# Kernel tuning notes

Measured on AMD Instinct MI355X. Metric: run time of the kernel, lower is better.

## Reference

```python
import jax, jax.numpy as jnp
import numpy as np

N = 262144        # tokens routed
D = 1024          # input_dim
E = 64            # num_experts
TOP_K = 2
NOISE_EPS = 1e-05
ALPHA = 10.0


def setup_inputs() -> dict:
    key = jax.random.key(0)
    k1, k2, k3, k4, k5 = jax.random.split(key, 5)
    x = jax.random.normal(k1, (N, D), dtype=jnp.float32)
    # nn.Linear init scale ~ 1/sqrt(fan_in); keep logits at sane magnitude
    gate_w = jax.random.normal(k2, (E, D), dtype=jnp.float32) * (1.0 / np.sqrt(D))
    gate_b = jax.random.normal(k3, (E,), dtype=jnp.float32) * 0.01
    # w_noise is initialized to zeros in the module; use small random values
    # so the noise path is exercised
    w_noise = jax.random.normal(k4, (E, E), dtype=jnp.float32) * 0.01
    noise = jax.random.normal(k5, (N, E), dtype=jnp.float32)  # torch.randn_like
    return {"x": x, "gate_w": gate_w, "gate_b": gate_b,
            "w_noise": w_noise, "noise": noise}


def reference(x, gate_w, gate_b, w_noise, noise):
    # gate linear: [N, D] @ [D, E] + [E]
    clean_logits = jnp.einsum('nd,ed->ne', x, gate_w) + gate_b
    # training-mode learnable noise injection
    raw_noise_stddev = clean_logits @ w_noise                 # [N, E]
    noise_stddev = jax.nn.softplus(raw_noise_stddev) + NOISE_EPS
    logits = clean_logits + noise * noise_stddev              # noisy_logits

    # decompostion_tp: k-th largest per row (kthvalue(n - k + 1) == k-th largest)
    kth_largest = jax.lax.top_k(logits, TOP_K)[0][:, -1]       # [N]
    mask = logits < kth_largest[:, None]                       # strictly below kth
    sm = jax.nn.softmax(logits, axis=1)
    out = jnp.where(mask,
                    ALPHA * jnp.log1p(sm),      # alpha * log(sm + 1)
                    ALPHA * jnp.expm1(sm))      # alpha * (exp(sm) - 1)

    gates = jax.nn.softmax(out, axis=1)
    return gates
```

## Files before the change

### kernel.cpp

```cpp
#include <hip/hip_runtime.h>

typedef _Float16 half8v __attribute__((ext_vector_type(8)));
typedef float f32x4 __attribute__((ext_vector_type(4)));

constexpr float INV4096 = 1.0f / 4096.0f;
constexpr float ALPHA = 10.0f;

__device__ __forceinline__ f32x4 mfma16(half8v a, half8v b, f32x4 c_) {
  return __builtin_amdgcn_mfma_f32_16x16x32_f16(a, b, c_, 0, 0, 0);
}

__device__ __forceinline__ void dma16(const void *g, void *l) {
  __builtin_amdgcn_global_load_lds(
      (const __attribute__((address_space(1))) void *)g,
      (__attribute__((address_space(3))) void *)l, 16, 0, 0);
}

__global__ __launch_bounds__(256) void presplit(const float *__restrict__ GW,
                                                const float *__restrict__ WN,
                                                char *__restrict__ ws) {
  const int b = blockIdx.x;
  const int tid = threadIdx.x;
  if (b < 64) {
    int idx = b * 256 + tid;
    int e = idx >> 8;
    int c4 = idx & 255;
    f32x4 v = *reinterpret_cast<const f32x4 *>(GW + (size_t)idx * 4);
#pragma unroll
    for (int j = 0; j < 4; ++j) {
      int k = c4 * 4 + j;
      float vv = v[j];
      _Float16 hh = (_Float16)vv;
      _Float16 ll = (_Float16)((vv - (float)hh) * 4096.0f);
      int ck = k >> 6, kk = k & 63;
      int off = ck * 16384 + e * 128 + ((((kk >> 3) ^ (e & 7))) << 4) + ((kk & 7) << 1);
      *reinterpret_cast<_Float16 *>(ws + off) = hh;
      *reinterpret_cast<_Float16 *>(ws + off + 8192) = ll;
    }
  } else {
    int idx = (b - 64) * 256 + tid;
    int k = idx >> 4;
    int e0 = (idx & 15) << 2;
    f32x4 v = *reinterpret_cast<const f32x4 *>(WN + (size_t)k * 64 + e0);
#pragma unroll
    for (int j = 0; j < 4; ++j) {
      int e = e0 + j;
      float vv = v[j];
      _Float16 hh = (_Float16)vv;
      _Float16 ll = (_Float16)((vv - (float)hh) * 4096.0f);
      int off = 262144 + e * 128 + ((((k >> 3) ^ (e & 7))) << 4) + ((k & 7) << 1);
      *reinterpret_cast<_Float16 *>(ws + off) = hh;
      *reinterpret_cast<_Float16 *>(ws + off + 8192) = ll;
    }
  }
}

__global__ __launch_bounds__(256, 3) void topk_gating(
    const float *__restrict__ X, const char *__restrict__ WS,
    const float *__restrict__ GB, const float *__restrict__ NZ,
    float *__restrict__ OUT) {
  __shared__ __align__(16) char lds[32768];
  const int tid = threadIdx.x;
  const int lane = tid & 63;
  const int wv = tid >> 6;
  const int q = lane >> 4;
  const int c = lane & 15;
  const int waveRow = blockIdx.x * 64 + wv * 16;

  f32x4 accH[4] = {};
  f32x4 accX[4] = {};
  f32x4 aCur[4], aNxt[4];

  const float *xBase = X + (size_t)(waveRow + c) * 1024 + q * 8;
  aCur[0] = *(const f32x4 *)(xBase + 0);
  aCur[1] = *(const f32x4 *)(xBase + 4);
  aCur[2] = *(const f32x4 *)(xBase + 32);
  aCur[3] = *(const f32x4 *)(xBase + 36);
#pragma unroll
  for (int i = 0; i < 4; ++i)
    dma16(WS + i * 4096 + wv * 1024 + lane * 16, lds + i * 4096 + wv * 1024);
  __syncthreads();

  for (int kc = 0; kc < 16; ++kc) {
    if (kc < 15) {
      const float *xb = xBase + (kc + 1) * 64;
      aNxt[0] = *(const f32x4 *)(xb + 0);
      aNxt[1] = *(const f32x4 *)(xb + 4);
      aNxt[2] = *(const f32x4 *)(xb + 32);
      aNxt[3] = *(const f32x4 *)(xb + 36);
      const int wbuf = ((kc + 1) & 1) * 16384;
      const char *src = WS + (kc + 1) * 16384;
#pragma unroll
      for (int i = 0; i < 4; ++i)
        dma16(src + i * 4096 + wv * 1024 + lane * 16,
              lds + wbuf + i * 4096 + wv * 1024);
    }
    const int buf = (kc & 1) * 16384;
#pragma unroll
    for (int ks = 0; ks < 2; ++ks) {
      half8v ah, al;
#pragma unroll
      for (int j = 0; j < 8; ++j) {
        float xv = aCur[ks * 2 + (j >> 2)][j & 3];
        _Float16 hh = (_Float16)xv;
        ah[j] = hh;
        al[j] = (_Float16)((xv - (float)hh) * 4096.0f);
      }
#pragma unroll
      for (int t = 0; t < 4; ++t) {
        int e = t * 16 + c;
        int off = buf + e * 128 + ((((ks * 4 + q) ^ (e & 7))) << 4);
        half8v bh = *reinterpret_cast<half8v *>(lds + off);
        half8v bl = *reinterpret_cast<half8v *>(lds + off + 8192);
        accH[t] = mfma16(ah, bh, accH[t]);
        accX[t] = mfma16(ah, bl, accX[t]);
        accX[t] = mfma16(al, bh, accX[t]);
      }
    }
    if (kc < 15) {
#pragma unroll
      for (int i = 0; i < 4; ++i) aCur[i] = aNxt[i];
    }
    __syncthreads();
  }

  float nz[4][4];
#pragma unroll
  for (int t = 0; t < 4; ++t)
#pragma unroll
    for (int r = 0; r < 4; ++r)
      nz[t][r] = NZ[(size_t)(waveRow + 4 * q + r) * 64 + t * 16 + c];

#pragma unroll
  for (int i = 0; i < 4; ++i)
    dma16(WS + 262144 + i * 4096 + wv * 1024 + lane * 16,
          lds + i * 4096 + wv * 1024);

  float cl[4][4];
#pragma unroll
  for (int t = 0; t < 4; ++t) {
    float bs = GB[t * 16 + c];
#pragma unroll
    for (int r = 0; r < 4; ++r)
      cl[t][r] = accH[t][r] + accX[t][r] * INV4096 + bs;
  }

  char *cb = lds + 16384 + wv * 4096;
#pragma unroll
  for (int t = 0; t < 4; ++t)
#pragma unroll
    for (int r = 0; r < 4; ++r) {
      int row = 4 * q + r;
      int colf = t * 16 + c;
      int off = row * 256 + ((((colf >> 2) ^ row)) << 4) + ((colf & 3) << 2);
      *reinterpret_cast<float *>(cb + off) = cl[t][r];
    }
  __syncthreads();

  f32x4 rH[4] = {};
  f32x4 rX[4] = {};
#pragma unroll
  for (int ks = 0; ks < 2; ++ks) {
    int slot0 = ks * 8 + q * 2;
    f32x4 a0 = *reinterpret_cast<f32x4 *>(cb + c * 256 + (((slot0 ^ c)) << 4));
    f32x4 a1 = *reinterpret_cast<f32x4 *>(cb + c * 256 + ((((slot0 + 1) ^ c)) << 4));
    half8v ah, al;
#pragma unroll
    for (int j = 0; j < 4; ++j) {
      float v = a0[j];
      _Float16 hh = (_Float16)v;
      ah[j] = hh;
      al[j] = (_Float16)((v - (float)hh) * 4096.0f);
      float v2 = a1[j];
      _Float16 h2 = (_Float16)v2;
      ah[4 + j] = h2;
      al[4 + j] = (_Float16)((v2 - (float)h2) * 4096.0f);
    }
#pragma unroll
    for (int t = 0; t < 4; ++t) {
      int e = t * 16 + c;
      int off = e * 128 + ((((ks * 4 + q) ^ (e & 7))) << 4);
      half8v bh = *reinterpret_cast<half8v *>(lds + off);
      half8v bl = *reinterpret_cast<half8v *>(lds + off + 8192);
      rH[t] = mfma16(ah, bh, rH[t]);
      rX[t] = mfma16(ah, bl, rX[t]);
      rX[t] = mfma16(al, bh, rX[t]);
    }
  }

  float lg[4][4];
#pragma unroll
  for (int t = 0; t < 4; ++t)
#pragma unroll
    for (int r = 0; r < 4; ++r) {
      float raw = rH[t][r] + rX[t][r] * INV4096;
      float sp = fmaxf(raw, 0.0f) + __logf(1.0f + __expf(-fabsf(raw)));
      lg[r][t] = cl[t][r] + nz[t][r] * (sp + 1e-5f);
    }

#pragma unroll
  for (int r = 0; r < 4; ++r) {
    float v0 = lg[r][0], v1 = lg[r][1], v2 = lg[r][2], v3 = lg[r][3];
    float a = fmaxf(v0, v1), b_ = fminf(v0, v1);
    float d1 = fmaxf(v2, v3), d2 = fminf(v2, v3);
    float m1 = fmaxf(a, d1);
    float m2 = fmaxf(fminf(a, d1), fmaxf(b_, d2));
#pragma unroll
    for (int s = 1; s <= 8; s <<= 1) {
      float om1 = __shfl_xor(m1, s, 64);
      float om2 = __shfl_xor(m2, s, 64);
      float hi = fmaxf(m1, om1);
      float lo = fminf(m1, om1);
      float sec = (m1 >= om1) ? m2 : om2;
      m2 = fmaxf(lo, sec);
      m1 = hi;
    }
    float se[4], ssum = 0.f;
#pragma unroll
    for (int t = 0; t < 4; ++t) {
      se[t] = __expf(lg[r][t] - m1);
      ssum += se[t];
    }
#pragma unroll
    for (int s = 1; s <= 8; s <<= 1) ssum += __shfl_xor(ssum, s, 64);
    float inv = 1.0f / ssum;
    float ov[4];
#pragma unroll
    for (int t = 0; t < 4; ++t) {
      float sm = se[t] * inv;
      float vlog = ALPHA * __logf(1.0f + sm);
      float vexp = ALPHA * (__expf(sm) - 1.0f);
      ov[t] = (lg[r][t] < m2) ? vlog : vexp;
    }
    float g = fmaxf(fmaxf(ov[0], ov[1]), fmaxf(ov[2], ov[3]));
#pragma unroll
    for (int s = 1; s <= 8; s <<= 1) g = fmaxf(g, __shfl_xor(g, s, 64));
    float gsum = 0.f;
#pragma unroll
    for (int t = 0; t < 4; ++t) {
      ov[t] = __expf(ov[t] - g);
      gsum += ov[t];
    }
#pragma unroll
    for (int s = 1; s <= 8; s <<= 1) gsum += __shfl_xor(gsum, s, 64);
    float ginv = 1.0f / gsum;
    size_t rowOff = (size_t)(waveRow + 4 * q + r) * 64;
#pragma unroll
    for (int t = 0; t < 4; ++t)
      OUT[rowOff + t * 16 + c] = ov[t] * ginv;
  }
}

extern "C" void kernel_launch(void *const *d_in, const int *in_sizes, int n_in,
                              void *d_out, int out_size, void *d_ws,
                              size_t ws_size, hipStream_t stream) {
  const float *x = (const float *)d_in[0];
  const float *gw = (const float *)d_in[1];
  const float *gb = (const float *)d_in[2];
  const float *wn = (const float *)d_in[3];
  const float *nz = (const float *)d_in[4];
  float *out = (float *)d_out;
  char *ws = (char *)d_ws;
  const int N = in_sizes[0] / 1024;

  hipLaunchKernelGGL(presplit, dim3(68), dim3(256), 0, stream, gw, wn, ws);
  hipLaunchKernelGGL(topk_gating, dim3(N / 64), dim3(256), 0, stream, x, ws,
                     gb, nz, out);
}
```

Baseline: 283.3 us.

## Deepen GEMM pipeline to triple-buffered LDS with explicit vmcnt waits

Replaces the double-buffered K loop with a fully unrolled three-stage pipeline. Weight chunks are DMA'd into LDS two steps ahead and X rows are prefetched three steps ahead into rotating register banks. The __syncthreads calls become raw s_barrier plus hand-counted s_waitcnt vmcnt so more loads stay in flight. This aims to hide global-memory latency in the memory-bound X stream. In exchange LDS grows to 48KB and register pressure rises, which may reduce occupancy, and the hand-counted vmcnt values are fragile if the compiler reorders loads.

```diff
diff --git a/kernel.cpp b/kernel.cpp
--- a/kernel.cpp
+++ b/kernel.cpp
@@ -9,11 +9,13 @@
 __device__ __forceinline__ f32x4 mfma16(half8v a, half8v b, f32x4 c_) {
   return __builtin_amdgcn_mfma_f32_16x16x32_f16(a, b, c_, 0, 0, 0);
 }
-
 __device__ __forceinline__ void dma16(const void *g, void *l) {
   __builtin_amdgcn_global_load_lds(
       (const __attribute__((address_space(1))) void *)g,
       (__attribute__((address_space(3))) void *)l, 16, 0, 0);
+}
+template <int N> __device__ __forceinline__ void wait_vm() {
+  asm volatile("s_waitcnt vmcnt(%0)" ::"n"(N) : "memory");
 }
 
 __global__ __launch_bounds__(256) void presplit(const float *__restrict__ GW,
@@ -59,7 +61,7 @@
     const float *__restrict__ X, const char *__restrict__ WS,
     const float *__restrict__ GB, const float *__restrict__ NZ,
     float *__restrict__ OUT) {
-  __shared__ __align__(16) char lds[32768];
+  __shared__ __align__(16) char lds[49152];
   const int tid = threadIdx.x;
   const int lane = tid & 63;
   const int wv = tid >> 6;
@@ -69,61 +71,88 @@
 
   f32x4 accH[4] = {};
   f32x4 accX[4] = {};
-  f32x4 aCur[4], aNxt[4];
+  f32x4 a0[4], a1[4], a2[4];
 
   const float *xBase = X + (size_t)(waveRow + c) * 1024 + q * 8;
-  aCur[0] = *(const f32x4 *)(xBase + 0);
-  aCur[1] = *(const f32x4 *)(xBase + 4);
-  aCur[2] = *(const f32x4 *)(xBase + 32);
-  aCur[3] = *(const f32x4 *)(xBase + 36);
+  const char *wsL = WS + wv * 1024 + lane * 16;
+  char *ldsL = lds + wv * 1024;
+
+#define LDA4(dst, p)                        \
+  {                                         \
+    dst[0] = *(const f32x4 *)((p) + 0);     \
+    dst[1] = *(const f32x4 *)((p) + 4);     \
+    dst[2] = *(const f32x4 *)((p) + 32);    \
+    dst[3] = *(const f32x4 *)((p) + 36);    \
+  }
+#define DMAB(CK)                                                            \
+  {                                                                         \
+    _Pragma("unroll") for (int i_ = 0; i_ < 4; ++i_)                        \
+        dma16(wsL + (CK) * 16384 + i_ * 4096,                               \
+              ldsL + ((CK) % 3) * 16384 + i_ * 4096);                       \
+  }
+#define CONV(A, ah, al)                                           \
+  {                                                               \
+    _Pragma("unroll") for (int ks_ = 0; ks_ < 2; ++ks_)           \
+        _Pragma("unroll") for (int j_ = 0; j_ < 8; ++j_) {        \
+      float xv_ = A[ks_ * 2 + (j_ >> 2)][j_ & 3];                 \
+      _Float16 hh_ = (_Float16)xv_;                               \
+      ah[ks_][j_] = hh_;                                          \
+      al[ks_][j_] = (_Float16)((xv_ - (float)hh_) * 4096.0f);     \
+    }                                                             \
+  }
+#define MFMAB(BUF, ah, al)                                                 \
+  {                                                                        \
+    _Pragma("unroll") for (int ks_ = 0; ks_ < 2; ++ks_)                    \
+        _Pragma("unroll") for (int t_ = 0; t_ < 4; ++t_) {                 \
+      int e_ = t_ * 16 + c;                                                \
+      int off_ = (BUF) + e_ * 128 + ((((ks_ * 4 + q) ^ (e_ & 7))) << 4);   \
+      half8v bh_ = *reinterpret_cast<half8v *>(lds + off_);                \
+      half8v bl_ = *reinterpret_cast<half8v *>(lds + off_ + 8192);         \
+      accH[t_] = mfma16(ah[ks_], bh_, accH[t_]);                           \
+      accX[t_] = mfma16(ah[ks_], bl_, accX[t_]);                           \
+      accX[t_] = mfma16(al[ks_], bh_, accX[t_]);                           \
+    }                                                                      \
+  }
+#define STEP(KC, ABANK)                                          \
+  {                                                              \
+    half8v ah[2], al[2];                                         \
+    CONV(ABANK, ah, al);                                         \
+    if ((KC) + 2 <= 15) DMAB((KC) + 2);                          \
+    if ((KC) + 3 <= 15) LDA4(ABANK, xBase + ((KC) + 3) * 64);    \
+    MFMAB(((KC) % 3) * 16384, ah, al);                           \
+  }
+#define BAR() __builtin_amdgcn_s_barrier()
+
+  DMAB(0);
+  DMAB(1);
+  LDA4(a0, xBase);
+  LDA4(a1, xBase + 64);
+  LDA4(a2, xBase + 128);
+  wait_vm<16>();
+  BAR();
+
+  STEP(0, a0)  wait_vm<12>(); BAR();
+  STEP(1, a1)  wait_vm<12>(); BAR();
+  STEP(2, a2)  wait_vm<12>(); BAR();
+  STEP(3, a0)  wait_vm<12>(); BAR();
+  STEP(4, a1)  wait_vm<12>(); BAR();
+  STEP(5, a2)  wait_vm<12>(); BAR();
+  STEP(6, a0)  wait_vm<12>(); BAR();
+  STEP(7, a1)  wait_vm<12>(); BAR();
+  STEP(8, a2)  wait_vm<12>(); BAR();
+  STEP(9, a0)  wait_vm<12>(); BAR();
+  STEP(10, a1) wait_vm<12>(); BAR();
+  STEP(11, a2) wait_vm<12>(); BAR();
+  STEP(12, a0) wait_vm<12>(); BAR();
+  STEP(13, a1) wait_vm<8>();  BAR();
+  STEP(14, a2) wait_vm<0>();  BAR();
+  STEP(15, a0)
+
+  float bs0 = GB[c], bs1 = GB[16 + c], bs2 = GB[32 + c], bs3 = GB[48 + c];
 #pragma unroll
   for (int i = 0; i < 4; ++i)
-    dma16(WS + i * 4096 + wv * 1024 + lane * 16, lds + i * 4096 + wv * 1024);
-  __syncthreads();
-
-  for (int kc = 0; kc < 16; ++kc) {
-    if (kc < 15) {
-      const float *xb = xBase + (kc + 1) * 64;
-      aNxt[0] = *(const f32x4 *)(xb + 0);
-      aNxt[1] = *(const f32x4 *)(xb + 4);
-      aNxt[2] = *(const f32x4 *)(xb + 32);
-      aNxt[3] = *(const f32x4 *)(xb + 36);
-      const int wbuf = ((kc + 1) & 1) * 16384;
-      const char *src = WS + (kc + 1) * 16384;
-#pragma unroll
-      for (int i = 0; i < 4; ++i)
-        dma16(src + i * 4096 + wv * 1024 + lane * 16,
-              lds + wbuf + i * 4096 + wv * 1024);
-    }
-    const int buf = (kc & 1) * 16384;
-#pragma unroll
-    for (int ks = 0; ks < 2; ++ks) {
-      half8v ah, al;
-#pragma unroll
-      for (int j = 0; j < 8; ++j) {
-        float xv = aCur[ks * 2 + (j >> 2)][j & 3];
-        _Float16 hh = (_Float16)xv;
-        ah[j] = hh;
-        al[j] = (_Float16)((xv - (float)hh) * 4096.0f);
-      }
-#pragma unroll
-      for (int t = 0; t < 4; ++t) {
-        int e = t * 16 + c;
-        int off = buf + e * 128 + ((((ks * 4 + q) ^ (e & 7))) << 4);
-        half8v bh = *reinterpret_cast<half8v *>(lds + off);
-        half8v bl = *reinterpret_cast<half8v *>(lds + off + 8192);
-        accH[t] = mfma16(ah, bh, accH[t]);
-        accX[t] = mfma16(ah, bl, accX[t]);
-        accX[t] = mfma16(al, bh, accX[t]);
-      }
-    }
-    if (kc < 15) {
-#pragma unroll
-      for (int i = 0; i < 4; ++i) aCur[i] = aNxt[i];
-    }
-    __syncthreads();
-  }
-
+    dma16(wsL + 262144 + i * 4096, ldsL + 16384 + i * 4096);
+  asm volatile("" ::: "memory");
   float nz[4][4];
 #pragma unroll
   for (int t = 0; t < 4; ++t)
@@ -131,21 +160,15 @@
     for (int r = 0; r < 4; ++r)
       nz[t][r] = NZ[(size_t)(waveRow + 4 * q + r) * 64 + t * 16 + c];
 
-#pragma unroll
-  for (int i = 0; i < 4; ++i)
-    dma16(WS + 262144 + i * 4096 + wv * 1024 + lane * 16,
-          lds + i * 4096 + wv * 1024);
-
   float cl[4][4];
-#pragma unroll
-  for (int t = 0; t < 4; ++t) {
-    float bs = GB[t * 16 + c];
+  const float bsv[4] = {bs0, bs1, bs2, bs3};
+#pragma unroll
+  for (int t = 0; t < 4; ++t)
 #pragma unroll
     for (int r = 0; r < 4; ++r)
-      cl[t][r] = accH[t][r] + accX[t][r] * INV4096 + bs;
-  }
-
-  char *cb = lds + 16384 + wv * 4096;
+      cl[t][r] = accH[t][r] + accX[t][r] * INV4096 + bsv[t];
+
+  char *cb = lds + 32768 + wv * 4096;
 #pragma unroll
   for (int t = 0; t < 4; ++t)
 #pragma unroll
@@ -155,23 +178,24 @@
       int off = row * 256 + ((((colf >> 2) ^ row)) << 4) + ((colf & 3) << 2);
       *reinterpret_cast<float *>(cb + off) = cl[t][r];
     }
-  __syncthreads();
+  wait_vm<16>();
+  BAR();
 
   f32x4 rH[4] = {};
   f32x4 rX[4] = {};
 #pragma unroll
   for (int ks = 0; ks < 2; ++ks) {
     int slot0 = ks * 8 + q * 2;
-    f32x4 a0 = *reinterpret_cast<f32x4 *>(cb + c * 256 + (((slot0 ^ c)) << 4));
-    f32x4 a1 = *reinterpret_cast<f32x4 *>(cb + c * 256 + ((((slot0 + 1) ^ c)) << 4));
+    f32x4 va = *reinterpret_cast<f32x4 *>(cb + c * 256 + (((slot0 ^ c)) << 4));
+    f32x4 vb = *reinterpret_cast<f32x4 *>(cb + c * 256 + ((((slot0 + 1) ^ c)) << 4));
     half8v ah, al;
 #pragma unroll
     for (int j = 0; j < 4; ++j) {
-      float v = a0[j];
+      float v = va[j];
       _Float16 hh = (_Float16)v;
       ah[j] = hh;
       al[j] = (_Float16)((v - (float)hh) * 4096.0f);
-      float v2 = a1[j];
+      float v2 = vb[j];
       _Float16 h2 = (_Float16)v2;
       ah[4 + j] = h2;
       al[4 + j] = (_Float16)((v2 - (float)h2) * 4096.0f);
@@ -179,7 +203,7 @@
 #pragma unroll
     for (int t = 0; t < 4; ++t) {
       int e = t * 16 + c;
-      int off = e * 128 + ((((ks * 4 + q) ^ (e & 7))) << 4);
+      int off = 16384 + e * 128 + ((((ks * 4 + q) ^ (e & 7))) << 4);
       half8v bh = *reinterpret_cast<half8v *>(lds + off);
       half8v bl = *reinterpret_cast<half8v *>(lds + off + 8192);
       rH[t] = mfma16(ah, bh, rH[t]);
```

After: 274.3 us. 3.2% less time.

## Load pre-laid-out gate weights directly into registers instead of LDS staging

Applied to the files above, without the earlier changes.

The presplit kernel now writes the fp16 hi/lo weight fragments in the exact per-lane MFMA operand order. The main kernel then loads B operands straight from global memory (L2-resident) into registers, with software prefetch across a fully unrolled K loop. This removes the LDS double buffer and the per-chunk __syncthreads, and halves LDS use, which may allow higher occupancy. The trade-offs are more VGPRs and redundant global/L2 traffic, since every wave re-reads the weights instead of sharing them through LDS.

```diff
diff --git a/kernel.cpp b/kernel.cpp
--- a/kernel.cpp
+++ b/kernel.cpp
@@ -8,50 +8,45 @@
 
 __device__ __forceinline__ f32x4 mfma16(half8v a, half8v b, f32x4 c_) {
   return __builtin_amdgcn_mfma_f32_16x16x32_f16(a, b, c_, 0, 0, 0);
-}
-
-__device__ __forceinline__ void dma16(const void *g, void *l) {
-  __builtin_amdgcn_global_load_lds(
-      (const __attribute__((address_space(1))) void *)g,
-      (__attribute__((address_space(3))) void *)l, 16, 0, 0);
 }
 
 __global__ __launch_bounds__(256) void presplit(const float *__restrict__ GW,
                                                 const float *__restrict__ WN,
                                                 char *__restrict__ ws) {
-  const int b = blockIdx.x;
-  const int tid = threadIdx.x;
-  if (b < 64) {
-    int idx = b * 256 + tid;
-    int e = idx >> 8;
-    int c4 = idx & 255;
-    f32x4 v = *reinterpret_cast<const f32x4 *>(GW + (size_t)idx * 4);
-#pragma unroll
-    for (int j = 0; j < 4; ++j) {
-      int k = c4 * 4 + j;
-      float vv = v[j];
+  const int gid = blockIdx.x * 256 + threadIdx.x;
+  if (gid < 8192) {
+    int e = gid >> 7, kp = gid & 127, k = kp * 8;
+    int kc = k >> 6, ks = (k >> 5) & 1, q = (k >> 3) & 3;
+    int t = e >> 4, lane = q * 16 + (e & 15);
+    const float *src = GW + (size_t)e * 1024 + k;
+    f32x4 v0 = *(const f32x4 *)src, v1 = *(const f32x4 *)(src + 4);
+    half8v h, l;
+#pragma unroll
+    for (int j = 0; j < 8; ++j) {
+      float vv = j < 4 ? v0[j] : v1[j - 4];
       _Float16 hh = (_Float16)vv;
-      _Float16 ll = (_Float16)((vv - (float)hh) * 4096.0f);
-      int ck = k >> 6, kk = k & 63;
-      int off = ck * 16384 + e * 128 + ((((kk >> 3) ^ (e & 7))) << 4) + ((kk & 7) << 1);
-      *reinterpret_cast<_Float16 *>(ws + off) = hh;
-      *reinterpret_cast<_Float16 *>(ws + off + 8192) = ll;
-    }
-  } else {
-    int idx = (b - 64) * 256 + tid;
-    int k = idx >> 4;
-    int e0 = (idx & 15) << 2;
-    f32x4 v = *reinterpret_cast<const f32x4 *>(WN + (size_t)k * 64 + e0);
-#pragma unroll
-    for (int j = 0; j < 4; ++j) {
-      int e = e0 + j;
-      float vv = v[j];
+      h[j] = hh;
+      l[j] = (_Float16)((vv - (float)hh) * 4096.0f);
+    }
+    size_t dst = (size_t)kc * 16384 + (ks * 4 + t) * 2048 + lane * 16;
+    *(half8v *)(ws + dst) = h;
+    *(half8v *)(ws + dst + 1024) = l;
+  } else if (gid < 8704) {
+    int idx = gid - 8192;
+    int e = idx >> 3, k = (idx & 7) * 8;
+    int ks = (k >> 5) & 1, q = (k >> 3) & 3;
+    int t = e >> 4, lane = q * 16 + (e & 15);
+    half8v h, l;
+#pragma unroll
+    for (int j = 0; j < 8; ++j) {
+      float vv = WN[(size_t)(k + j) * 64 + e];
       _Float16 hh = (_Float16)vv;
-      _Float16 ll = (_Float16)((vv - (float)hh) * 4096.0f);
-      int off = 262144 + e * 128 + ((((k >> 3) ^ (e & 7))) << 4) + ((k & 7) << 1);
-      *reinterpret_cast<_Float16 *>(ws + off) = hh;
-      *reinterpret_cast<_Float16 *>(ws + off + 8192) = ll;
-    }
+      h[j] = hh;
+      l[j] = (_Float16)((vv - (float)hh) * 4096.0f);
+    }
+    size_t dst = 262144 + (size_t)(ks * 4 + t) * 2048 + lane * 16;
+    *(half8v *)(ws + dst) = h;
+    *(half8v *)(ws + dst + 1024) = l;
   }
 }
 
@@ -59,71 +54,90 @@
     const float *__restrict__ X, const char *__restrict__ WS,
     const float *__restrict__ GB, const float *__restrict__ NZ,
     float *__restrict__ OUT) {
-  __shared__ __align__(16) char lds[32768];
-  const int tid = threadIdx.x;
-  const int lane = tid & 63;
-  const int wv = tid >> 6;
-  const int q = lane >> 4;
-  const int c = lane & 15;
+  __shared__ __align__(16) char lds[16384];
+  const int tid = threadIdx.x, lane = tid & 63, wv = tid >> 6;
+  const int q = lane >> 4, c = lane & 15;
   const int waveRow = blockIdx.x * 64 + wv * 16;
-
-  f32x4 accH[4] = {};
-  f32x4 accX[4] = {};
-  f32x4 aCur[4], aNxt[4];
-
   const float *xBase = X + (size_t)(waveRow + c) * 1024 + q * 8;
-  aCur[0] = *(const f32x4 *)(xBase + 0);
-  aCur[1] = *(const f32x4 *)(xBase + 4);
-  aCur[2] = *(const f32x4 *)(xBase + 32);
-  aCur[3] = *(const f32x4 *)(xBase + 36);
-#pragma unroll
-  for (int i = 0; i < 4; ++i)
-    dma16(WS + i * 4096 + wv * 1024 + lane * 16, lds + i * 4096 + wv * 1024);
-  __syncthreads();
-
-  for (int kc = 0; kc < 16; ++kc) {
-    if (kc < 15) {
-      const float *xb = xBase + (kc + 1) * 64;
-      aNxt[0] = *(const f32x4 *)(xb + 0);
-      aNxt[1] = *(const f32x4 *)(xb + 4);
-      aNxt[2] = *(const f32x4 *)(xb + 32);
-      aNxt[3] = *(const f32x4 *)(xb + 36);
-      const int wbuf = ((kc + 1) & 1) * 16384;
-      const char *src = WS + (kc + 1) * 16384;
-#pragma unroll
-      for (int i = 0; i < 4; ++i)
-        dma16(src + i * 4096 + wv * 1024 + lane * 16,
-              lds + wbuf + i * 4096 + wv * 1024);
-    }
-    const int buf = (kc & 1) * 16384;
-#pragma unroll
-    for (int ks = 0; ks < 2; ++ks) {
-      half8v ah, al;
-#pragma unroll
-      for (int j = 0; j < 8; ++j) {
-        float xv = aCur[ks * 2 + (j >> 2)][j & 3];
-        _Float16 hh = (_Float16)xv;
-        ah[j] = hh;
-        al[j] = (_Float16)((xv - (float)hh) * 4096.0f);
-      }
-#pragma unroll
-      for (int t = 0; t < 4; ++t) {
-        int e = t * 16 + c;
-        int off = buf + e * 128 + ((((ks * 4 + q) ^ (e & 7))) << 4);
-        half8v bh = *reinterpret_cast<half8v *>(lds + off);
-        half8v bl = *reinterpret_cast<half8v *>(lds + off + 8192);
-        accH[t] = mfma16(ah, bh, accH[t]);
-        accX[t] = mfma16(ah, bl, accX[t]);
-        accX[t] = mfma16(al, bh, accX[t]);
-      }
-    }
-    if (kc < 15) {
-#pragma unroll
-      for (int i = 0; i < 4; ++i) aCur[i] = aNxt[i];
-    }
-    __syncthreads();
-  }
-
+  const char *wsF = WS + lane * 16;
+
+  f32x4 accH[4] = {}, accX[4] = {};
+  f32x4 aA[4], aB[4];
+  half8v b0h[4], b0l[4], b1h[4], b1l[4];
+
+#define LDA4(dst, p)                     \
+  {                                      \
+    dst[0] = *(const f32x4 *)((p));      \
+    dst[1] = *(const f32x4 *)((p) + 4);  \
+    dst[2] = *(const f32x4 *)((p) + 32); \
+    dst[3] = *(const f32x4 *)((p) + 36); \
+  }
+#define LDB(KC, KS, BH, BL)                                        \
+  {                                                                \
+    _Pragma("unroll") for (int t_ = 0; t_ < 4; ++t_) {             \
+      const char *p_ = wsF + (KC)*16384 + ((KS)*4 + t_) * 2048;    \
+      BH[t_] = *(const half8v *)p_;                                \
+      BL[t_] = *(const half8v *)(p_ + 1024);                       \
+    }                                                              \
+  }
+#define CONV(A, ah, al)                                       \
+  {                                                           \
+    _Pragma("unroll") for (int ks_ = 0; ks_ < 2; ++ks_)       \
+        _Pragma("unroll") for (int j_ = 0; j_ < 8; ++j_) {    \
+      float xv_ = A[ks_ * 2 + (j_ >> 2)][j_ & 3];             \
+      _Float16 hh_ = (_Float16)xv_;                           \
+      ah[ks_][j_] = hh_;                                      \
+      al[ks_][j_] = (_Float16)((xv_ - (float)hh_) * 4096.0f); \
+    }                                                         \
+  }
+#define MF(AH, AL, BH, BL)                             \
+  {                                                    \
+    _Pragma("unroll") for (int t_ = 0; t_ < 4; ++t_) { \
+      accH[t_] = mfma16(AH, BH[t_], accH[t_]);         \
+      accX[t_] = mfma16(AH, BL[t_], accX[t_]);         \
+      accX[t_] = mfma16(AL, BH[t_], accX[t_]);         \
+    }                                                  \
+  }
+#define STEP(KC, ACUR, ANXT)                                \
+  {                                                         \
+    if ((KC) + 1 < 16) LDA4(ANXT, xBase + ((KC) + 1) * 64); \
+    half8v ah[2], al[2];                                    \
+    CONV(ACUR, ah, al);                                     \
+    LDB((KC), 1, b1h, b1l);                                 \
+    MF(ah[0], al[0], b0h, b0l);                             \
+    if ((KC) + 1 < 16) LDB((KC) + 1, 0, b0h, b0l);          \
+    MF(ah[1], al[1], b1h, b1l);                             \
+  }
+
+  LDA4(aA, xBase);
+  LDB(0, 0, b0h, b0l);
+  STEP(0, aA, aB)
+  STEP(1, aB, aA)
+  STEP(2, aA, aB)
+  STEP(3, aB, aA)
+  STEP(4, aA, aB)
+  STEP(5, aB, aA)
+  STEP(6, aA, aB)
+  STEP(7, aB, aA)
+  STEP(8, aA, aB)
+  STEP(9, aB, aA)
+  STEP(10, aA, aB)
+  STEP(11, aB, aA)
+  STEP(12, aA, aB)
+  STEP(13, aB, aA)
+  STEP(14, aA, aB)
+  STEP(15, aB, aA)
+
+  float bs0 = GB[c], bs1 = GB[16 + c], bs2 = GB[32 + c], bs3 = GB[48 + c];
+  half8v wnh[8], wnl[8];
+#pragma unroll
+  for (int ks = 0; ks < 2; ++ks)
+#pragma unroll
+    for (int t = 0; t < 4; ++t) {
+      const char *p = wsF + 262144 + (ks * 4 + t) * 2048;
+      wnh[ks * 4 + t] = *(const half8v *)p;
+      wnl[ks * 4 + t] = *(const half8v *)(p + 1024);
+    }
   float nz[4][4];
 #pragma unroll
   for (int t = 0; t < 4; ++t)
@@ -131,21 +145,15 @@
     for (int r = 0; r < 4; ++r)
       nz[t][r] = NZ[(size_t)(waveRow + 4 * q + r) * 64 + t * 16 + c];
 
-#pragma unroll
-  for (int i = 0; i < 4; ++i)
-    dma16(WS + 262144 + i * 4096 + wv * 1024 + lane * 16,
-          lds + i * 4096 + wv * 1024);
-
   float cl[4][4];
-#pragma unroll
-  for (int t = 0; t < 4; ++t) {
-    float bs = GB[t * 16 + c];
+  const float bsv[4] = {bs0, bs1, bs2, bs3};
+#pragma unroll
+  for (int t = 0; t < 4; ++t)
 #pragma unroll
     for (int r = 0; r < 4; ++r)
-      cl[t][r] = accH[t][r] + accX[t][r] * INV4096 + bs;
-  }
-
-  char *cb = lds + 16384 + wv * 4096;
+      cl[t][r] = accH[t][r] + accX[t][r] * INV4096 + bsv[t];
+
+  char *cb = lds + wv * 4096;
 #pragma unroll
   for (int t = 0; t < 4; ++t)
 #pragma unroll
@@ -155,36 +163,32 @@
       int off = row * 256 + ((((colf >> 2) ^ row)) << 4) + ((colf & 3) << 2);
       *reinterpret_cast<float *>(cb + off) = cl[t][r];
     }
-  __syncthreads();
 
   f32x4 rH[4] = {};
   f32x4 rX[4] = {};
 #pragma unroll
   for (int ks = 0; ks < 2; ++ks) {
     int slot0 = ks * 8 + q * 2;
-    f32x4 a0 = *reinterpret_cast<f32x4 *>(cb + c * 256 + (((slot0 ^ c)) << 4));
-    f32x4 a1 = *reinterpret_cast<f32x4 *>(cb + c * 256 + ((((slot0 + 1) ^ c)) << 4));
+    f32x4 va = *reinterpret_cast<f32x4 *>(cb + c * 256 + (((slot0 ^ c)) << 4));
+    f32x4 vb =
+        *reinterpret_cast<f32x4 *>(cb + c * 256 + ((((slot0 + 1) ^ c)) << 4));
     half8v ah, al;
 #pragma unroll
     for (int j = 0; j < 4; ++j) {
-      float v = a0[j];
+      float v = va[j];
       _Float16 hh = (_Float16)v;
       ah[j] = hh;
       al[j] = (_Float16)((v - (float)hh) * 4096.0f);
-      float v2 = a1[j];
+      float v2 = vb[j];
       _Float16 h2 = (_Float16)v2;
       ah[4 + j] = h2;
       al[4 + j] = (_Float16)((v2 - (float)h2) * 4096.0f);
     }
 #pragma unroll
     for (int t = 0; t < 4; ++t) {
-      int e = t * 16 + c;
-      int off = e * 128 + ((((ks * 4 + q) ^ (e & 7))) << 4);
-      half8v bh = *reinterpret_cast<half8v *>(lds + off);
-      half8v bl = *reinterpret_cast<half8v *>(lds + off + 8192);
-      rH[t] = mfma16(ah, bh, rH[t]);
-      rX[t] = mfma16(ah, bl, rX[t]);
-      rX[t] = mfma16(al, bh, rX[t]);
+      rH[t] = mfma16(ah, wnh[ks * 4 + t], rH[t]);
+      rX[t] = mfma16(ah, wnl[ks * 4 + t], rX[t]);
+      rX[t] = mfma16(al, wnh[ks * 4 + t], rX[t]);
     }
   }
 
@@ -263,7 +267,7 @@
   char *ws = (char *)d_ws;
   const int N = in_sizes[0] / 1024;
 
-  hipLaunchKernelGGL(presplit, dim3(68), dim3(256), 0, stream, gw, wn, ws);
+  hipLaunchKernelGGL(presplit, dim3(34), dim3(256), 0, stream, gw, wn, ws);
   hipLaunchKernelGGL(topk_gating, dim3(N / 64), dim3(256), 0, stream, x, ws,
                      gb, nz, out);
 }
```

Result: slower. 439.9 us (+55.3%).
